# Optimization experiments

Measured on AMD Instinct MI355X. Metric: run time of the kernel, lower is better.

## Reference

```python
import jax, jax.numpy as jnp
import numpy as np
from jax import lax

BATCH, SEQ, IN_F, H_SIZE, OUT_F = 65536, 64, 16, 10, 5

def setup_inputs() -> dict:
    key = jax.random.key(0)
    k1, k2, k3, k4, k5 = jax.random.split(key, 5)
    x = jax.random.uniform(k1, (BATCH, SEQ, IN_F), dtype=jnp.float32)
    W1 = jax.random.normal(k2, (IN_F, H_SIZE), dtype=jnp.float32) * (1.0 / np.sqrt(IN_F))
    b1 = jax.random.normal(k3, (H_SIZE,), dtype=jnp.float32) * 0.02
    W2 = jax.random.normal(k4, (H_SIZE, OUT_F), dtype=jnp.float32) * (1.0 / np.sqrt(H_SIZE))
    b2 = jax.random.normal(k5, (OUT_F,), dtype=jnp.float32) * 0.02
    return {"x": x, "W1": W1, "b1": b1, "W2": W2, "b2": b2}

def reference(x, W1, b1, W2, b2):
    # h_{t} = tanh(h_{t-1} + x_t @ W1 + b1); y = sigmoid(h_T @ W2 + b2)
    b = x.shape[0]
    h0 = jnp.zeros((b, W1.shape[1]), dtype=x.dtype)
    # precompute all input projections in one big GEMM: [B,S,H]
    a = jnp.einsum('bsi,ih->bsh', x, W1) + b1
    def step(h, a_t):
        return jnp.tanh(h + a_t), None
    h, _ = lax.scan(step, h0, jnp.swapaxes(a, 0, 1))  # scan over seq
    return jax.nn.sigmoid(h @ W2 + b2)
```

## Files before the change

### kernel.cpp

```cpp
#include <hip/hip_runtime.h>

#define BATCH 65536
#define SEQ   64
#define INF   16
#define HS    10
#define OUTF  5

#define PIN(v) asm volatile("" : "+v"(v))

__global__ __launch_bounds__(256, 1) void rnn_fused(
    const float* __restrict__ x,  const float* __restrict__ W1,
    const float* __restrict__ b1, const float* __restrict__ W2,
    const float* __restrict__ b2, float* __restrict__ out)
{
    const int b = blockIdx.x * 256 + threadIdx.x;

    float w1[INF * HS];
#pragma unroll
    for (int k = 0; k < INF * HS; ++k) { w1[k] = W1[k]; }
#pragma unroll
    for (int k = 0; k < INF * HS; ++k) { PIN(w1[k]); }

    float bb1[HS];
#pragma unroll
    for (int h = 0; h < HS; ++h) { bb1[h] = b1[h]; }
#pragma unroll
    for (int h = 0; h < HS; ++h) { PIN(bb1[h]); }

    float hreg[HS];
#pragma unroll
    for (int h = 0; h < HS; ++h) hreg[h] = 0.0f;

    const float4* __restrict__ xr =
        reinterpret_cast<const float4*>(x + (size_t)b * (SEQ * INF));

    float4 buf[4][4];
#pragma unroll
    for (int r = 0; r < 4; ++r)
#pragma unroll
        for (int j = 0; j < 4; ++j) buf[r][j] = xr[r * 4 + j];

#pragma unroll 4
    for (int s = 0; s < SEQ; ++s) {
        const int slot = s & 3;
        float xv[INF];
#pragma unroll
        for (int j = 0; j < 4; ++j) {
            xv[j * 4 + 0] = buf[slot][j].x;
            xv[j * 4 + 1] = buf[slot][j].y;
            xv[j * 4 + 2] = buf[slot][j].z;
            xv[j * 4 + 3] = buf[slot][j].w;
        }
        const int pf = (s + 4 < SEQ) ? (s + 4) : (SEQ - 1);
#pragma unroll
        for (int j = 0; j < 4; ++j) buf[slot][j] = xr[pf * 4 + j];

        float a[HS];
#pragma unroll
        for (int h = 0; h < HS; ++h) a[h] = bb1[h];
#pragma unroll
        for (int i = 0; i < INF; ++i)
#pragma unroll
            for (int h = 0; h < HS; ++h)
                a[h] = fmaf(xv[i], w1[i * HS + h], a[h]);

#pragma unroll
        for (int h = 0; h < HS; ++h) {
            float t = hreg[h] + a[h];
            float e = __expf(2.0f * t);
            hreg[h] = fmaf(-2.0f, __builtin_amdgcn_rcpf(e + 1.0f), 1.0f);
        }
    }

    float y[OUTF];
#pragma unroll
    for (int o = 0; o < OUTF; ++o) y[o] = b2[o];
#pragma unroll
    for (int h = 0; h < HS; ++h)
#pragma unroll
        for (int o = 0; o < OUTF; ++o)
            y[o] = fmaf(hreg[h], W2[h * OUTF + o], y[o]);

    float* op = out + (size_t)b * OUTF;
#pragma unroll
    for (int o = 0; o < OUTF; ++o)
        op[o] = __builtin_amdgcn_rcpf(1.0f + __expf(-y[o]));
}

extern "C" void kernel_launch(void* const* d_in, const int* in_sizes, int n_in,
                              void* d_out, int out_size, void* d_ws, size_t ws_size,
                              hipStream_t stream) {
    const float* x  = (const float*)d_in[0];
    const float* W1 = (const float*)d_in[1];
    const float* b1 = (const float*)d_in[2];
    const float* W2 = (const float*)d_in[3];
    const float* b2 = (const float*)d_in[4];
    float* out = (float*)d_out;

    rnn_fused<<<BATCH / 256, 256, 0, stream>>>(x, W1, b1, W2, b2, out);
}
```

Measured before the change: 434.3 us.

## Split each batch row across four lanes with shuffle reduction

Each batch row is now handled by four consecutive lanes, each owning four input features and a slice of W1. Partial projections are combined with two xor shuffles, so all four lanes keep the full hidden state. Adjacent lanes now read adjacent float4s, which coalesces the x loads, and lower per-thread register use allows higher occupancy. In exchange, each step adds shuffles and the tanh work is repeated on all four lanes.

```diff
diff --git a/kernel.cpp b/kernel.cpp
--- a/kernel.cpp
+++ b/kernel.cpp
@@ -8,61 +8,62 @@
 
 #define PIN(v) asm volatile("" : "+v"(v))
 
-__global__ __launch_bounds__(256, 1) void rnn_fused(
+__global__ __launch_bounds__(256, 4) void rnn_fused(
     const float* __restrict__ x,  const float* __restrict__ W1,
     const float* __restrict__ b1, const float* __restrict__ W2,
     const float* __restrict__ b2, float* __restrict__ out)
 {
-    const int b = blockIdx.x * 256 + threadIdx.x;
+    const int g   = blockIdx.x * 256 + threadIdx.x;
+    const int row = g >> 2;
+    const int j   = g & 3;
 
-    float w1[INF * HS];
+    float w1l[4 * HS];
 #pragma unroll
-    for (int k = 0; k < INF * HS; ++k) { w1[k] = W1[k]; }
+    for (int il = 0; il < 4; ++il)
 #pragma unroll
-    for (int k = 0; k < INF * HS; ++k) { PIN(w1[k]); }
+        for (int h = 0; h < HS; ++h)
+            w1l[il * HS + h] = W1[(4 * j + il) * HS + h];
+#pragma unroll
+    for (int k = 0; k < 4 * HS; ++k) { PIN(w1l[k]); }
 
-    float bb1[HS];
+    float bq[HS];
 #pragma unroll
-    for (int h = 0; h < HS; ++h) { bb1[h] = b1[h]; }
+    for (int h = 0; h < HS; ++h) { bq[h] = 0.25f * b1[h]; }
 #pragma unroll
-    for (int h = 0; h < HS; ++h) { PIN(bb1[h]); }
+    for (int h = 0; h < HS; ++h) { PIN(bq[h]); }
 
     float hreg[HS];
 #pragma unroll
     for (int h = 0; h < HS; ++h) hreg[h] = 0.0f;
 
     const float4* __restrict__ xr =
-        reinterpret_cast<const float4*>(x + (size_t)b * (SEQ * INF));
+        reinterpret_cast<const float4*>(x) + (size_t)row * (SEQ * 4) + j;
 
-    float4 buf[4][4];
+    float4 buf[4];
 #pragma unroll
-    for (int r = 0; r < 4; ++r)
-#pragma unroll
-        for (int j = 0; j < 4; ++j) buf[r][j] = xr[r * 4 + j];
+    for (int r = 0; r < 4; ++r) buf[r] = xr[r * 4];
 
 #pragma unroll 4
     for (int s = 0; s < SEQ; ++s) {
         const int slot = s & 3;
-        float xv[INF];
-#pragma unroll
-        for (int j = 0; j < 4; ++j) {
-            xv[j * 4 + 0] = buf[slot][j].x;
-            xv[j * 4 + 1] = buf[slot][j].y;
-            xv[j * 4 + 2] = buf[slot][j].z;
-            xv[j * 4 + 3] = buf[slot][j].w;
-        }
+        const float4 xv = buf[slot];
         const int pf = (s + 4 < SEQ) ? (s + 4) : (SEQ - 1);
-#pragma unroll
-        for (int j = 0; j < 4; ++j) buf[slot][j] = xr[pf * 4 + j];
+        buf[slot] = xr[pf * 4];
 
         float a[HS];
 #pragma unroll
-        for (int h = 0; h < HS; ++h) a[h] = bb1[h];
+        for (int h = 0; h < HS; ++h) a[h] = bq[h];
 #pragma unroll
-        for (int i = 0; i < INF; ++i)
+        for (int h = 0; h < HS; ++h) {
+            a[h] = fmaf(xv.x, w1l[0 * HS + h], a[h]);
+            a[h] = fmaf(xv.y, w1l[1 * HS + h], a[h]);
+            a[h] = fmaf(xv.z, w1l[2 * HS + h], a[h]);
+            a[h] = fmaf(xv.w, w1l[3 * HS + h], a[h]);
+        }
 #pragma unroll
-            for (int h = 0; h < HS; ++h)
-                a[h] = fmaf(xv[i], w1[i * HS + h], a[h]);
+        for (int h = 0; h < HS; ++h) a[h] += __shfl_xor(a[h], 1);
+#pragma unroll
+        for (int h = 0; h < HS; ++h) a[h] += __shfl_xor(a[h], 2);
 
 #pragma unroll
         for (int h = 0; h < HS; ++h) {
@@ -80,11 +81,13 @@
 #pragma unroll
         for (int o = 0; o < OUTF; ++o)
             y[o] = fmaf(hreg[h], W2[h * OUTF + o], y[o]);
-
-    float* op = out + (size_t)b * OUTF;
 #pragma unroll
     for (int o = 0; o < OUTF; ++o)
-        op[o] = __builtin_amdgcn_rcpf(1.0f + __expf(-y[o]));
+        y[o] = __builtin_amdgcn_rcpf(1.0f + __expf(-y[o]));
+
+    float* op = out + (size_t)row * OUTF;
+    op[j] = y[j];
+    if (j == 0) op[4] = y[4];
 }
 
 extern "C" void kernel_launch(void* const* d_in, const int* in_sizes, int n_in,
@@ -97,5 +100,5 @@
     const float* b2 = (const float*)d_in[4];
     float* out = (float*)d_out;
 
-    rnn_fused<<<BATCH / 256, 256, 0, stream>>>(x, W1, b1, W2, b2, out);
+    rnn_fused<<<(BATCH * 4) / 256, 256, 0, stream>>>(x, W1, b1, W2, b2, out);
 }
```

Measured after the change: 396.1 us. -8.8%, faster.
